# Kernel tuning notes

Hardware: AMD Instinct MI355X
Metric: run time of the kernel (lower is better)

Reference implementation:

```python
import jax, jax.numpy as jnp
import numpy as np

N_NODES = 100000
N_EDGES = 3200000
HIDDEN = 64
OUT = 30


def _graph_conv(x, src, dst, W, b, n_nodes):
    # DGL GraphConv with norm='both': D_out^{-1/2} -> aggregate -> D_in^{-1/2} -> W -> +b
    ones = jnp.ones(src.shape[0], dtype=x.dtype)
    deg_out = jax.ops.segment_sum(ones, src, num_segments=n_nodes)
    deg_in = jax.ops.segment_sum(ones, dst, num_segments=n_nodes)
    norm_out = jnp.where(deg_out > 0, jax.lax.rsqrt(jnp.maximum(deg_out, 1e-30)), 0.0)
    norm_in = jnp.where(deg_in > 0, jax.lax.rsqrt(jnp.maximum(deg_in, 1e-30)), 0.0)
    h = x * norm_out[:, None]                    # [N, F] scaled source features
    msg = h[src]                                 # [E, F] gather
    agg = jax.ops.segment_sum(msg, dst, num_segments=n_nodes)  # [N, F] scatter-add
    agg = agg * norm_in[:, None]
    return agg @ W + b


def setup_inputs() -> dict:
    key = jax.random.key(0)
    k1, k2, k3, k4, k5 = jax.random.split(key, 5)
    x = jax.random.normal(k1, (N_NODES, HIDDEN), dtype=jnp.float32)
    src = jax.random.randint(k2, (N_EDGES,), 0, N_NODES, dtype=jnp.int32)
    dst = jax.random.randint(k3, (N_EDGES,), 0, N_NODES, dtype=jnp.int32)
    W1 = jax.random.normal(k4, (HIDDEN, HIDDEN), dtype=jnp.float32) / np.sqrt(HIDDEN)
    b1 = jnp.zeros((HIDDEN,), dtype=jnp.float32)
    W2 = jax.random.normal(k5, (HIDDEN, OUT), dtype=jnp.float32) / np.sqrt(HIDDEN)
    b2 = jnp.zeros((OUT,), dtype=jnp.float32)
    return {"x": x, "src": src, "dst": dst, "W1": W1, "b1": b1, "W2": W2, "b2": b2}


def reference(x, src, dst, W1, b1, W2, b2):
    h = _graph_conv(x, src, dst, W1, b1, N_NODES)
    h = jax.nn.relu(h)                           # conv1 activation=F.relu
    out = _graph_conv(h, src, dst, W2, b2, N_NODES)  # conv2: no activation
    return out
```

## Files before the change

### kernel.cpp

```cpp
#include <hip/hip_runtime.h>


#define NN 100000
#define NE 3200000
#define NOUTF 30
#define TPB 256
#define TPBW 1024
#define TPBS 512

#define DSH 8
#define DCB 256
#define DNB ((NN + DCB - 1) / DCB)
#define SSH 10
#define SCB 1024
#define SNB ((NN + SCB - 1) / SCB)

#define CHUNK 8192
#define NBLK ((NE + CHUNK - 1) / CHUNK)
#define HLD (DNB * NBLK)
#define HLS (SNB * NBLK)
#define HLT (HLD + HLS)
#define EPT (CHUNK / TPBS)

#define GCH 1024
#define NSC ((HLT + GCH - 1) / GCH)

#define POOL 9216

__device__ __forceinline__ unsigned short f2bf(float f) {
  unsigned u = __float_as_uint(f);
  u = (u + 0x7FFFu + ((u >> 16) & 1u)) >> 16;
  return (unsigned short)u;
}

__device__ __forceinline__ void acc8(float* a, const uint4& u) {
  a[0] += __uint_as_float(u.x << 16);
  a[1] += __uint_as_float(u.x & 0xFFFF0000u);
  a[2] += __uint_as_float(u.y << 16);
  a[3] += __uint_as_float(u.y & 0xFFFF0000u);
  a[4] += __uint_as_float(u.z << 16);
  a[5] += __uint_as_float(u.z & 0xFFFF0000u);
  a[6] += __uint_as_float(u.w << 16);
  a[7] += __uint_as_float(u.w & 0xFFFF0000u);
}

__device__ __forceinline__ uint4 sel4(bool ok, uint4 u) {
  uint4 z = make_uint4(0u, 0u, 0u, 0u);
  return ok ? u : z;
}

__device__ __forceinline__ int xcd_swz(int orig, int n) {
  int q = n / 8, r = n % 8;
  int xcd = orig % 8, idx = orig / 8;
  return (xcd < r ? xcd * (q + 1) : r * (q + 1) + (xcd - r) * q) + idx;
}

__global__ __launch_bounds__(TPBW) void k_hist(const int* __restrict__ src,
                                               const int* __restrict__ dst,
                                               int* __restrict__ H) {
  __shared__ int hd[DNB], hs[SNB];
  int t = threadIdx.x, k = blockIdx.x;
  for (int b = t; b < DNB; b += TPBW) hd[b] = 0;
  for (int b = t; b < SNB; b += TPBW) hs[b] = 0;
  __syncthreads();
  int beg = k * CHUNK, end = min(NE, beg + CHUNK);
  for (int i = beg + t; i < end; i += TPBW) {
    atomicAdd(&hd[dst[i] >> DSH], 1);
    atomicAdd(&hs[src[i] >> SSH], 1);
  }
  __syncthreads();
  for (int b = t; b < DNB; b += TPBW) H[b * NBLK + k] = hd[b];
  for (int b = t; b < SNB; b += TPBW) H[HLD + b * NBLK + k] = hs[b];
}

__global__ __launch_bounds__(TPB) void g_scan1(const int* __restrict__ a,
                                               int* __restrict__ bsums) {
  int t = threadIdx.x;
  int base = blockIdx.x * GCH + t * 4;
  int s = 0;
#pragma unroll
  for (int j = 0; j < 4; ++j) { int idx = base + j; if (idx < HLT) s += a[idx]; }
  __shared__ int red[TPB];
  red[t] = s; __syncthreads();
  for (int off = TPB / 2; off > 0; off >>= 1) {
    if (t < off) red[t] += red[t + off];
    __syncthreads();
  }
  if (t == 0) bsums[blockIdx.x] = red[0];
}

__global__ __launch_bounds__(1024) void g_scan2(int* __restrict__ bsums) {
  int t = threadIdx.x;
  __shared__ int lds[1024];
  int v = (t < NSC) ? bsums[t] : 0;
  int acc = v; lds[t] = acc; __syncthreads();
  for (int off = 1; off < 1024; off <<= 1) {
    int add = (t >= off) ? lds[t - off] : 0; __syncthreads();
    acc += add; lds[t] = acc; __syncthreads();
  }
  if (t < NSC) bsums[t] = acc - v;
}

__global__ __launch_bounds__(TPB) void g_scan3(int* __restrict__ a,
                                               const int* __restrict__ bsums) {
  int t = threadIdx.x;
  int base = blockIdx.x * GCH + t * 4;
  int v[4]; int s = 0;
#pragma unroll
  for (int j = 0; j < 4; ++j) {
    int idx = base + j;
    v[j] = (idx < HLT) ? a[idx] : 0;
    s += v[j];
  }
  __shared__ int lds[TPB];
  int acc = s; lds[t] = acc; __syncthreads();
  for (int off = 1; off < TPB; off <<= 1) {
    int add = (t >= off) ? lds[t - off] : 0; __syncthreads();
    acc += add; lds[t] = acc; __syncthreads();
  }
  int run = bsums[blockIdx.x] + (acc - s);
#pragma unroll
  for (int j = 0; j < 4; ++j) {
    int idx = base + j;
    if (idx < HLT) a[idx] = run;
    run += v[j];
  }
}

__global__ __launch_bounds__(TPBS) void k_scatter(const int* __restrict__ src,
                                                  const int* __restrict__ dst,
                                                  const int* __restrict__ Hsc,
                                                  int* __restrict__ packed,
                                                  unsigned short* __restrict__ ss) {
  __shared__ int pack_lds[CHUNK];
  __shared__ unsigned short ss_lds[CHUNK];
  __shared__ int baseD[DNB + 1], curD[DNB];
  __shared__ int baseS[SNB + 1], curS[SNB];
  __shared__ int scanbuf[TPBS];
  int t = threadIdx.x;
  int k = xcd_swz((int)blockIdx.x, NBLK);
  int beg = k * CHUNK, end = min(NE, beg + CHUNK);
  int cnt = end - beg;

  int es[EPT], ed[EPT];
#pragma unroll
  for (int j = 0; j < EPT; ++j) {
    int i = beg + j * TPBS + t;
    if (i < end) { es[j] = src[i]; ed[j] = dst[i]; }
    else { es[j] = -1; ed[j] = -1; }
  }

  for (int b = t; b < DNB; b += TPBS) curD[b] = 0;
  for (int b = t; b < SNB; b += TPBS) curS[b] = 0;
  __syncthreads();
#pragma unroll
  for (int j = 0; j < EPT; ++j) {
    if (ed[j] >= 0) {
      atomicAdd(&curD[ed[j] >> DSH], 1);
      atomicAdd(&curS[es[j] >> SSH], 1);
    }
  }
  __syncthreads();

  {
    int v = (t < DNB) ? curD[t] : 0;
    int acc = v; scanbuf[t] = acc; __syncthreads();
    for (int off = 1; off < TPBS; off <<= 1) {
      int add = (t >= off) ? scanbuf[t - off] : 0; __syncthreads();
      acc += add; scanbuf[t] = acc; __syncthreads();
    }
    if (t < DNB) baseD[t] = acc - v;
    if (t == 0) baseD[DNB] = cnt;
  }
  __syncthreads();
  {
    int v = (t < SNB) ? curS[t] : 0;
    int acc = v; scanbuf[t] = acc; __syncthreads();
    for (int off = 1; off < TPBS; off <<= 1) {
      int add = (t >= off) ? scanbuf[t - off] : 0; __syncthreads();
      acc += add; scanbuf[t] = acc; __syncthreads();
    }
    if (t < SNB) baseS[t] = acc - v;
    if (t == 0) baseS[SNB] = cnt;
  }
  __syncthreads();
  for (int b = t; b < DNB; b += TPBS) curD[b] = baseD[b];
  for (int b = t; b < SNB; b += TPBS) curS[b] = baseS[b];
  __syncthreads();

#pragma unroll
  for (int j = 0; j < EPT; ++j) {
    if (ed[j] >= 0) {
      int p = atomicAdd(&curD[ed[j] >> DSH], 1);
      pack_lds[p] = (es[j] << DSH) | (ed[j] & (DCB - 1));
      int q = atomicAdd(&curS[es[j] >> SSH], 1);
      ss_lds[q] = (unsigned short)(es[j] & (SCB - 1));
    }
  }
  __syncthreads();

  for (int i = t; i < cnt; i += TPBS) {
    int lo = 0, hi = DNB;
    while (hi - lo > 1) { int mid = (lo + hi) >> 1; if (baseD[mid] <= i) lo = mid; else hi = mid; }
    packed[Hsc[lo * NBLK + k] + (i - baseD[lo])] = pack_lds[i];
  }
  for (int i = t; i < cnt; i += TPBS) {
    int lo = 0, hi = SNB;
    while (hi - lo > 1) { int mid = (lo + hi) >> 1; if (baseS[mid] <= i) lo = mid; else hi = mid; }
    ss[Hsc[HLD + lo * NBLK + k] + (i - baseS[lo]) - NE] = ss_lds[i];
  }
}

__global__ __launch_bounds__(TPB) void k_fine_sort(const int* __restrict__ Hsc,
                                                   const int* __restrict__ packed,
                                                   int* __restrict__ src_sorted,
                                                   int* __restrict__ row_ptr,
                                                   float* __restrict__ norm_in) {
  __shared__ int hist[DCB], scn[DCB], cur[DCB];
  __shared__ int pool[POOL];
  int t = threadIdx.x, b = blockIdx.x;
  int seg_beg = Hsc[b * NBLK];
  int seg_end = (b + 1 < DNB) ? Hsc[(b + 1) * NBLK] : NE;
  int cnt = seg_end - seg_beg;
  hist[t] = 0;
  __syncthreads();
  for (int i = seg_beg + t; i < seg_end; i += TPB)
    atomicAdd(&hist[packed[i] & (DCB - 1)], 1);
  __syncthreads();
  scn[t] = hist[t];
  __syncthreads();
  for (int off = 1; off < DCB; off <<= 1) {
    int add = (t >= off) ? scn[t - off] : 0;
    __syncthreads();
    scn[t] += add;
    __syncthreads();
  }
  {
    int excl = scn[t] - hist[t];
    cur[t] = excl;
    int node = b * DCB + t;
    if (node < NN) {
      row_ptr[node] = seg_beg + excl;
      norm_in[node] = (hist[t] > 0) ? rsqrtf((float)hist[t]) : 0.0f;
    }
  }
  if (b == DNB - 1 && t == 0) row_ptr[NN] = NE;
  __syncthreads();
  for (int i = seg_beg + t; i < seg_end; i += TPB) {
    int v = packed[i];
    int p = atomicAdd(&cur[v & (DCB - 1)], 1);
    int sv = v >> DSH;
    if (p < POOL) pool[p] = sv;
    else src_sorted[seg_beg + p] = sv;
  }
  __syncthreads();
  int lim = min(cnt, POOL);
  for (int i = t; i < lim; i += TPB) src_sorted[seg_beg + i] = pool[i];
}

__global__ __launch_bounds__(TPB) void k_fine_count(const int* __restrict__ Hsc,
                                                    const unsigned short* __restrict__ ss,
                                                    float* __restrict__ norm_out) {
  __shared__ int hist[SCB];
  int t = threadIdx.x, b = blockIdx.x;
  int seg_beg = Hsc[HLD + b * NBLK] - NE;
  int seg_end = (b + 1 < SNB) ? Hsc[HLD + (b + 1) * NBLK] - NE : NE;
  for (int i = t; i < SCB; i += TPB) hist[i] = 0;
  __syncthreads();
  for (int i = seg_beg + t; i < seg_end; i += TPB)
    atomicAdd(&hist[ss[i]], 1);
  __syncthreads();
  for (int i = t; i < SCB; i += TPB) {
    int node = b * SCB + i;
    if (node < NN)
      norm_out[node] = (hist[i] > 0) ? rsqrtf((float)hist[i]) : 0.0f;
  }
}

__global__ __launch_bounds__(TPB) void k_gemm1(const float4* __restrict__ x4,
                                               const float* __restrict__ W1,
                                               const float* __restrict__ norm_out,
                                               unsigned short* __restrict__ xt_b) {
  int lane = threadIdx.x & 63;
  int wid = (blockIdx.x * TPB + threadIdx.x) >> 6;
  int nwaves = gridDim.x * (TPB / 64);
  float w[64];
#pragma unroll
  for (int k = 0; k < 64; ++k) w[k] = W1[k * 64 + lane];
  int m = lane >> 4, q = lane & 15;
  for (int grp = wid; grp < NN / 4; grp += nwaves) {
    int nbase = grp * 4;
    float4 rv = x4[(nbase + m) * 16 + q];
    int r0 = __float_as_int(rv.x), r1 = __float_as_int(rv.y);
    int r2 = __float_as_int(rv.z), r3 = __float_as_int(rv.w);
    float acc[4] = {0.f, 0.f, 0.f, 0.f};
#pragma unroll
    for (int mm = 0; mm < 4; ++mm) {
#pragma unroll
      for (int ql = 0; ql < 16; ++ql) {
        int sl = mm * 16 + ql;
        acc[mm] = fmaf(__int_as_float(__builtin_amdgcn_readlane(r0, sl)), w[ql * 4 + 0], acc[mm]);
        acc[mm] = fmaf(__int_as_float(__builtin_amdgcn_readlane(r1, sl)), w[ql * 4 + 1], acc[mm]);
        acc[mm] = fmaf(__int_as_float(__builtin_amdgcn_readlane(r2, sl)), w[ql * 4 + 2], acc[mm]);
        acc[mm] = fmaf(__int_as_float(__builtin_amdgcn_readlane(r3, sl)), w[ql * 4 + 3], acc[mm]);
      }
    }
#pragma unroll
    for (int mm = 0; mm < 4; ++mm) {
      int n = nbase + mm;
      xt_b[n * 64 + lane] = f2bf(norm_out[n] * acc[mm]);
    }
  }
}

__global__ __launch_bounds__(TPB) void k_agg1f(const uint4* __restrict__ xt4,
                                               const int* __restrict__ src_sorted,
                                               const int* __restrict__ row_ptr,
                                               const float* __restrict__ norm_in,
                                               const float* __restrict__ norm_out,
                                               const float* __restrict__ b1,
                                               const float* __restrict__ W2,
                                               unsigned short* __restrict__ h1t_b) {
  __shared__ __align__(16) float h1s[4][64];
  __shared__ float W2s[64][32];
  int t = threadIdx.x;
  for (int i = t; i < 64 * NOUTF; i += TPB)
    W2s[i / NOUTF][i % NOUTF] = W2[i];

  int w = t >> 6;
  int lane = t & 63;
  int node = blockIdx.x * 4 + w;
  int slot = lane >> 3;
  int fl = lane & 7;
  int beg = row_ptr[node];
  int end = row_ptr[node + 1];
  float a[8] = {0.f, 0.f, 0.f, 0.f, 0.f, 0.f, 0.f, 0.f};
  if (beg < end) {
    int last = end - 1;
    for (int e = beg + slot; e < end; e += 32) {
      int e1 = min(e + 8, last), e2 = min(e + 16, last), e3 = min(e + 24, last);
      bool k1 = (e + 8) < end, k2 = (e + 16) < end, k3 = (e + 24) < end;
      int s0 = src_sorted[e], s1 = src_sorted[e1];
      int s2 = src_sorted[e2], s3 = src_sorted[e3];
      uint4 u0 = xt4[s0 * 8 + fl];
      uint4 u1 = xt4[s1 * 8 + fl];
      uint4 u2 = xt4[s2 * 8 + fl];
      uint4 u3 = xt4[s3 * 8 + fl];
      u1 = sel4(k1, u1); u2 = sel4(k2, u2); u3 = sel4(k3, u3);
      acc8(a, u0); acc8(a, u1); acc8(a, u2); acc8(a, u3);
    }
  }
#pragma unroll
  for (int off = 8; off <= 32; off <<= 1) {
#pragma unroll
    for (int j = 0; j < 8; ++j) a[j] += __shfl_xor(a[j], off);
  }
  if (slot == 0) {
    float ni = norm_in[node];
    float4 blo = reinterpret_cast<const float4*>(b1)[fl * 2];
    float4 bhi = reinterpret_cast<const float4*>(b1)[fl * 2 + 1];
    float4 r0, r1;
    r0.x = fmaxf(fmaf(a[0], ni, blo.x), 0.f);
    r0.y = fmaxf(fmaf(a[1], ni, blo.y), 0.f);
    r0.z = fmaxf(fmaf(a[2], ni, blo.z), 0.f);
    r0.w = fmaxf(fmaf(a[3], ni, blo.w), 0.f);
    r1.x = fmaxf(fmaf(a[4], ni, bhi.x), 0.f);
    r1.y = fmaxf(fmaf(a[5], ni, bhi.y), 0.f);
    r1.z = fmaxf(fmaf(a[6], ni, bhi.z), 0.f);
    r1.w = fmaxf(fmaf(a[7], ni, bhi.w), 0.f);
    *reinterpret_cast<float4*>(&h1s[w][fl * 8]) = r0;
    *reinterpret_cast<float4*>(&h1s[w][fl * 8 + 4]) = r1;
  }
  __syncthreads();
  if (t < 128) {
    int wn = t >> 5, oc = t & 31;
    int n = blockIdx.x * 4 + wn;
    if (oc < NOUTF) {
      float a0 = 0.f, a1 = 0.f, a2 = 0.f, a3 = 0.f;
#pragma unroll
      for (int k = 0; k < 64; k += 4) {
        a0 = fmaf(h1s[wn][k],     W2s[k][oc],     a0);
        a1 = fmaf(h1s[wn][k + 1], W2s[k + 1][oc], a1);
        a2 = fmaf(h1s[wn][k + 2], W2s[k + 2][oc], a2);
        a3 = fmaf(h1s[wn][k + 3], W2s[k + 3][oc], a3);
      }
      h1t_b[n * 32 + oc] = f2bf(norm_out[n] * ((a0 + a1) + (a2 + a3)));
    } else {
      h1t_b[n * 32 + oc] = 0;
    }
  }
}

__global__ __launch_bounds__(TPB) void k_agg2(const uint4* __restrict__ h1t4,
                                              const int* __restrict__ src_sorted,
                                              const int* __restrict__ row_ptr,
                                              const float* __restrict__ norm_in,
                                              const float* __restrict__ b2,
                                              float* __restrict__ out) {
  int node = (blockIdx.x * TPB + threadIdx.x) >> 6;
  int lane = threadIdx.x & 63;
  int slot = lane >> 2;
  int fl = lane & 3;
  int beg = row_ptr[node];
  int end = row_ptr[node + 1];
  float a[8] = {0.f, 0.f, 0.f, 0.f, 0.f, 0.f, 0.f, 0.f};
  int e = beg + slot;
  for (; e + 16 < end; e += 32) {
    int s0 = src_sorted[e];
    int s1 = src_sorted[e + 16];
    uint4 u0 = h1t4[s0 * 4 + fl];
    uint4 u1 = h1t4[s1 * 4 + fl];
    acc8(a, u0);
    acc8(a, u1);
  }
  if (e < end) {
    uint4 u0 = h1t4[src_sorted[e] * 4 + fl];
    acc8(a, u0);
  }
#pragma unroll
  for (int off = 4; off <= 32; off <<= 1) {
#pragma unroll
    for (int j = 0; j < 8; ++j) a[j] += __shfl_xor(a[j], off);
  }
  if (slot == 0) {
    float ni = norm_in[node];
    int f0 = fl * 8;
    float2* ob = (float2*)(out + (size_t)node * NOUTF);
#pragma unroll
    for (int p = 0; p < 4; ++p) {
      int f = f0 + p * 2;
      if (f < NOUTF) {
        float2 v;
        v.x = fmaf(a[p * 2], ni, b2[f]);
        v.y = fmaf(a[p * 2 + 1], ni, b2[f + 1]);
        ob[f >> 1] = v;
      }
    }
  }
}

extern "C" void kernel_launch(void* const* d_in, const int* in_sizes, int n_in,
                              void* d_out, int out_size, void* d_ws, size_t ws_size,
                              hipStream_t stream) {
  (void)in_sizes; (void)n_in; (void)out_size; (void)ws_size;
  const float* x = (const float*)d_in[0];
  const int* src = (const int*)d_in[1];
  const int* dst = (const int*)d_in[2];
  const float* W1 = (const float*)d_in[3];
  const float* b1 = (const float*)d_in[4];
  const float* W2 = (const float*)d_in[5];
  const float* b2 = (const float*)d_in[6];
  float* out = (float*)d_out;

  char* ws = (char*)d_ws;
  int* row_ptr = (int*)(ws + 0);
  float* norm_out = (float*)(ws + 400128);
  float* norm_in = (float*)(ws + 800128);
  int* H = (int*)(ws + 1200128);
  int* bsums = (int*)(ws + 1964928);
  unsigned short* ss = (unsigned short*)(ws + 1965696);
  int* src_sorted = (int*)(ws + 8365696);
  int* packed = (int*)(ws + 21165696);
  unsigned short* h1t_b = (unsigned short*)(ws + 21165696);
  unsigned short* xt_b = (unsigned short*)(ws + 46765696);

  k_hist<<<NBLK, TPBW, 0, stream>>>(src, dst, H);
  g_scan1<<<NSC, TPB, 0, stream>>>(H, bsums);
  g_scan2<<<1, 1024, 0, stream>>>(bsums);
  g_scan3<<<NSC, TPB, 0, stream>>>(H, bsums);
  k_scatter<<<NBLK, TPBS, 0, stream>>>(src, dst, H, packed, ss);
  k_fine_sort<<<DNB, TPB, 0, stream>>>(H, packed, src_sorted, row_ptr, norm_in);
  k_fine_count<<<SNB, TPB, 0, stream>>>(H, ss, norm_out);
  k_gemm1<<<1024, TPB, 0, stream>>>((const float4*)x, W1, norm_out, xt_b);
  k_agg1f<<<NN / 4, TPB, 0, stream>>>((const uint4*)xt_b, src_sorted, row_ptr,
                                      norm_in, norm_out, b1, W2, h1t_b);
  k_agg2<<<NN / 4, TPB, 0, stream>>>((const uint4*)h1t_b, src_sorted, row_ptr, norm_in, b2, out);
}
```

Before: 260.4 us.

## Make agg1 a persistent wave-per-node loop with in-register W2 projection

The first aggregation kernel becomes a grid-stride persistent kernel with a fixed block count. Each wave loops over nodes, so the W2 tile is loaded into shared memory once per block instead of once per four nodes. The 64-to-30 projection now runs inside each wave using shuffles, replacing the shared-memory staging buffer and block barrier. The edge loop is unrolled by two instead of four with a tail, which lowers per-thread memory-level parallelism but removes the clamped padded loads.

```diff
diff --git a/kernel.cpp b/kernel.cpp
--- a/kernel.cpp
+++ b/kernel.cpp
@@ -7,6 +7,7 @@
 #define TPB 256
 #define TPBW 1024
 #define TPBS 512
+#define AGG1_BLOCKS 2048
 
 #define DSH 8
 #define DCB 256
@@ -42,11 +43,6 @@
   a[5] += __uint_as_float(u.z & 0xFFFF0000u);
   a[6] += __uint_as_float(u.w << 16);
   a[7] += __uint_as_float(u.w & 0xFFFF0000u);
-}
-
-__device__ __forceinline__ uint4 sel4(bool ok, uint4 u) {
-  uint4 z = make_uint4(0u, 0u, 0u, 0u);
-  return ok ? u : z;
 }
 
 __device__ __forceinline__ int xcd_swz(int orig, int n) {
@@ -321,72 +317,66 @@
                                                const float* __restrict__ b1,
                                                const float* __restrict__ W2,
                                                unsigned short* __restrict__ h1t_b) {
-  __shared__ __align__(16) float h1s[4][64];
   __shared__ float W2s[64][32];
   int t = threadIdx.x;
-  for (int i = t; i < 64 * NOUTF; i += TPB)
-    W2s[i / NOUTF][i % NOUTF] = W2[i];
-
-  int w = t >> 6;
+  for (int i = t; i < 64 * 32; i += TPB) {
+    int r = i >> 5, c = i & 31;
+    W2s[r][c] = (c < NOUTF) ? W2[r * NOUTF + c] : 0.f;
+  }
+  __syncthreads();
+
   int lane = t & 63;
-  int node = blockIdx.x * 4 + w;
   int slot = lane >> 3;
   int fl = lane & 7;
-  int beg = row_ptr[node];
-  int end = row_ptr[node + 1];
-  float a[8] = {0.f, 0.f, 0.f, 0.f, 0.f, 0.f, 0.f, 0.f};
-  if (beg < end) {
-    int last = end - 1;
-    for (int e = beg + slot; e < end; e += 32) {
-      int e1 = min(e + 8, last), e2 = min(e + 16, last), e3 = min(e + 24, last);
-      bool k1 = (e + 8) < end, k2 = (e + 16) < end, k3 = (e + 24) < end;
-      int s0 = src_sorted[e], s1 = src_sorted[e1];
-      int s2 = src_sorted[e2], s3 = src_sorted[e3];
+  int oc = lane & 31;
+  int half = lane & 32;
+  int gwave = (blockIdx.x * TPB + t) >> 6;
+  int nwaves = gridDim.x * (TPB / 64);
+
+  const float4* b1_4 = reinterpret_cast<const float4*>(b1);
+  float4 bl = b1_4[fl * 2];
+  float4 bh = b1_4[fl * 2 + 1];
+  float b1r[8] = {bl.x, bl.y, bl.z, bl.w, bh.x, bh.y, bh.z, bh.w};
+
+  for (int node = gwave; node < NN; node += nwaves) {
+    int beg = row_ptr[node];
+    int end = row_ptr[node + 1];
+    float a[8] = {0.f, 0.f, 0.f, 0.f, 0.f, 0.f, 0.f, 0.f};
+    int e = beg + slot;
+    for (; e + 8 < end; e += 16) {
+      int s0 = src_sorted[e];
+      int s1 = src_sorted[e + 8];
       uint4 u0 = xt4[s0 * 8 + fl];
       uint4 u1 = xt4[s1 * 8 + fl];
-      uint4 u2 = xt4[s2 * 8 + fl];
-      uint4 u3 = xt4[s3 * 8 + fl];
-      u1 = sel4(k1, u1); u2 = sel4(k2, u2); u3 = sel4(k3, u3);
-      acc8(a, u0); acc8(a, u1); acc8(a, u2); acc8(a, u3);
-    }
-  }
-#pragma unroll
-  for (int off = 8; off <= 32; off <<= 1) {
-#pragma unroll
-    for (int j = 0; j < 8; ++j) a[j] += __shfl_xor(a[j], off);
-  }
-  if (slot == 0) {
+      acc8(a, u0);
+      acc8(a, u1);
+    }
+    if (e < end) {
+      uint4 u0 = xt4[src_sorted[e] * 8 + fl];
+      acc8(a, u0);
+    }
+#pragma unroll
+    for (int off = 8; off <= 32; off <<= 1) {
+#pragma unroll
+      for (int j = 0; j < 8; ++j) a[j] += __shfl_xor(a[j], off);
+    }
     float ni = norm_in[node];
-    float4 blo = reinterpret_cast<const float4*>(b1)[fl * 2];
-    float4 bhi = reinterpret_cast<const float4*>(b1)[fl * 2 + 1];
-    float4 r0, r1;
-    r0.x = fmaxf(fmaf(a[0], ni, blo.x), 0.f);
-    r0.y = fmaxf(fmaf(a[1], ni, blo.y), 0.f);
-    r0.z = fmaxf(fmaf(a[2], ni, blo.z), 0.f);
-    r0.w = fmaxf(fmaf(a[3], ni, blo.w), 0.f);
-    r1.x = fmaxf(fmaf(a[4], ni, bhi.x), 0.f);
-    r1.y = fmaxf(fmaf(a[5], ni, bhi.y), 0.f);
-    r1.z = fmaxf(fmaf(a[6], ni, bhi.z), 0.f);
-    r1.w = fmaxf(fmaf(a[7], ni, bhi.w), 0.f);
-    *reinterpret_cast<float4*>(&h1s[w][fl * 8]) = r0;
-    *reinterpret_cast<float4*>(&h1s[w][fl * 8 + 4]) = r1;
-  }
-  __syncthreads();
-  if (t < 128) {
-    int wn = t >> 5, oc = t & 31;
-    int n = blockIdx.x * 4 + wn;
-    if (oc < NOUTF) {
-      float a0 = 0.f, a1 = 0.f, a2 = 0.f, a3 = 0.f;
-#pragma unroll
-      for (int k = 0; k < 64; k += 4) {
-        a0 = fmaf(h1s[wn][k],     W2s[k][oc],     a0);
-        a1 = fmaf(h1s[wn][k + 1], W2s[k + 1][oc], a1);
-        a2 = fmaf(h1s[wn][k + 2], W2s[k + 2][oc], a2);
-        a3 = fmaf(h1s[wn][k + 3], W2s[k + 3][oc], a3);
-      }
-      h1t_b[n * 32 + oc] = f2bf(norm_out[n] * ((a0 + a1) + (a2 + a3)));
-    } else {
-      h1t_b[n * 32 + oc] = 0;
+    float no = norm_out[node];
+#pragma unroll
+    for (int j = 0; j < 8; ++j)
+      a[j] = fmaxf(fmaf(a[j], ni, b1r[j]), 0.f);
+
+    float accv = 0.f;
+#pragma unroll
+    for (int kk = 0; kk < 32; ++kk) {
+      int f = kk + half;
+      float hv = __shfl(a[kk & 7], f >> 3);
+      accv = fmaf(hv, W2s[f][oc], accv);
+    }
+    accv += __shfl_xor(accv, 32);
+    if (lane < 32) {
+      unsigned short v = (oc < NOUTF) ? f2bf(no * accv) : (unsigned short)0;
+      h1t_b[node * 32 + oc] = v;
     }
   }
 }
@@ -472,7 +462,7 @@
   k_fine_sort<<<DNB, TPB, 0, stream>>>(H, packed, src_sorted, row_ptr, norm_in);
   k_fine_count<<<SNB, TPB, 0, stream>>>(H, ss, norm_out);
   k_gemm1<<<1024, TPB, 0, stream>>>((const float4*)x, W1, norm_out, xt_b);
-  k_agg1f<<<NN / 4, TPB, 0, stream>>>((const uint4*)xt_b, src_sorted, row_ptr,
-                                      norm_in, norm_out, b1, W2, h1t_b);
+  k_agg1f<<<AGG1_BLOCKS, TPB, 0, stream>>>((const uint4*)xt_b, src_sorted, row_ptr,
+                                           norm_in, norm_out, b1, W2, h1t_b);
   k_agg2<<<NN / 4, TPB, 0, stream>>>((const uint4*)h1t_b, src_sorted, row_ptr, norm_in, b2, out);
 }
```

New measurement: 284.6 us. +9.3%, slower.
